# Optimization experiments

Measured on AMD Instinct MI355X. Metric: run time of the kernel, lower is better.

The kernel has to match this reference:

```python
import jax, jax.numpy as jnp
import numpy as np

EPS = 1e-7  # keras K.epsilon()


def setup_inputs() -> dict:
    key = jax.random.key(0)
    k1, k2, k3, k4 = jax.random.split(key, 4)
    B, Lc, La, Dc, Da = 64, 512, 64, 1024, 1024
    return {
        "context": jax.random.normal(k1, (B, Lc, Dc), dtype=jnp.float32),
        "asp_text": jax.random.normal(k2, (B, La, Da), dtype=jnp.float32),
        "context_w": jax.random.normal(k3, (Dc, Da), dtype=jnp.float32) / np.sqrt(Dc),
        "context_b": jnp.zeros((Lc,), dtype=jnp.float32),
        "aspect_w": jax.random.normal(k4, (Da, Dc), dtype=jnp.float32) / np.sqrt(Da),
        "aspect_b": jnp.zeros((La,), dtype=jnp.float32),
    }


def reference(context, asp_text, context_w, context_b, aspect_w, aspect_b):
    # context: [B, Lc, Dc], asp_text: [B, La, Da]
    context_avg = jnp.mean(context, axis=1)   # [B, Dc]
    asp_avg = jnp.mean(asp_text, axis=1)      # [B, Da]

    # context attention scored against mean-pooled aspect
    s_c = jnp.einsum('bld,de,be->bl', context, context_w, asp_avg)  # [B, Lc]
    a_c = jnp.exp(jnp.tanh(s_c + context_b))
    a_c = a_c / (jnp.sum(a_c, axis=1, keepdims=True) + EPS)
    attend_context = jnp.einsum('bld,bl->bd', context, a_c)         # [B, Dc]

    # aspect attention scored against mean-pooled context
    s_t = jnp.einsum('bld,de,be->bl', asp_text, aspect_w, context_avg)  # [B, La]
    a_t = jnp.exp(jnp.tanh(s_t + aspect_b))
    # NOTE: faithful to original code's bug -- a_t is REPLACED by its sum
    # (not normalized), so the aspect branch scales sum(asp_text) by a scalar.
    a_t_sum = jnp.sum(a_t, axis=1, keepdims=True) + EPS              # [B, 1]
    attend_asp = jnp.sum(asp_text * a_t_sum[..., None], axis=1)      # [B, Da]

    return jnp.concatenate([attend_context, attend_asp], axis=-1)    # [B, Dc+Da]
```

## Files before the change

kernel.cpp:

```cpp
#include <hip/hip_runtime.h>
#include <hip/hip_bf16.h>

#define EPS 1e-7f

#define B   64
#define LC  512
#define LA  64
#define D   1024
#define D4  256
#define ROWS 16
#define CCHUNKS (LC / ROWS)

__global__ void k_asp_psum(const float* __restrict__ A, float* __restrict__ P) {
    int b = blockIdx.y, s = blockIdx.x, t = threadIdx.x;
    const float4* Ab = reinterpret_cast<const float4*>(A + (size_t)b * LA * D);
    float sx = 0.f, sy = 0.f, sz = 0.f, sw = 0.f;
    #pragma unroll
    for (int r = 0; r < ROWS; ++r) {
        float4 v = Ab[(s * ROWS + r) * D4 + t];
        sx += v.x; sy += v.y; sz += v.z; sw += v.w;
    }
    float4 o; o.x = sx; o.y = sy; o.z = sz; o.w = sw;
    reinterpret_cast<float4*>(P)[(b * 4 + s) * D4 + t] = o;
}

__global__ void k_asp_combine(const float* __restrict__ P, float* __restrict__ avg) {
    int b = blockIdx.x, t = threadIdx.x;
    const float4* P4 = reinterpret_cast<const float4*>(P);
    float sx = 0.f, sy = 0.f, sz = 0.f, sw = 0.f;
    #pragma unroll
    for (int s = 0; s < 4; ++s) {
        float4 v = P4[(b * 4 + s) * D4 + t];
        sx += v.x; sy += v.y; sz += v.z; sw += v.w;
    }
    const float inv = 1.0f / (float)LA;
    float4 o; o.x = sx * inv; o.y = sy * inv; o.z = sz * inv; o.w = sw * inv;
    reinterpret_cast<float4*>(avg)[b * D4 + t] = o;
}

__global__ void k_matvec(const float* __restrict__ W, const float* __restrict__ X,
                         float* __restrict__ V) {
    int w    = threadIdx.x >> 6;
    int lane = threadIdx.x & 63;
    int d0   = (blockIdx.x * 4 + w) * 2;
    int b0   = blockIdx.y * 16;

    float4 w0[4], w1[4];
    const float4* Wr0 = reinterpret_cast<const float4*>(W + (size_t)d0 * D);
    const float4* Wr1 = reinterpret_cast<const float4*>(W + (size_t)(d0 + 1) * D);
    #pragma unroll
    for (int k = 0; k < 4; ++k) { w0[k] = Wr0[lane + 64 * k]; w1[k] = Wr1[lane + 64 * k]; }

    #pragma unroll 4
    for (int bb = 0; bb < 16; ++bb) {
        int b = b0 + bb;
        const float4* Xr = reinterpret_cast<const float4*>(X + (size_t)b * D);
        float p0 = 0.f, p1 = 0.f;
        #pragma unroll
        for (int k = 0; k < 4; ++k) {
            float4 x = Xr[lane + 64 * k];
            p0 += x.x * w0[k].x + x.y * w0[k].y + x.z * w0[k].z + x.w * w0[k].w;
            p1 += x.x * w1[k].x + x.y * w1[k].y + x.z * w1[k].z + x.w * w1[k].w;
        }
        #pragma unroll
        for (int m = 1; m < 64; m <<= 1) {
            p0 += __shfl_xor(p0, m, 64);
            p1 += __shfl_xor(p1, m, 64);
        }
        if (lane == 0) { V[b * D + d0] = p0; V[b * D + d0 + 1] = p1; }
    }
}

__global__ __launch_bounds__(256, 4)
void k_ctx_pass(const float* __restrict__ C, const float* __restrict__ vc,
                const float* __restrict__ cb,
                float* __restrict__ pacc, float* __restrict__ psum,
                float* __restrict__ pesum) {
    __shared__ float sdot[ROWS][4];
    __shared__ float se[ROWS];
    int b = blockIdx.y, c = blockIdx.x;
    int w    = threadIdx.x >> 6;
    int lane = threadIdx.x & 63;
    int f4   = w * 64 + lane;

    float4 vr = reinterpret_cast<const float4*>(vc + (size_t)b * D)[f4];

    const float4* Cb = reinterpret_cast<const float4*>(C + ((size_t)b * LC + c * ROWS) * D);
    float4 x[ROWS];
    #pragma unroll
    for (int r = 0; r < ROWS; ++r) x[r] = Cb[r * D4 + f4];

    #pragma unroll
    for (int r = 0; r < ROWS; ++r) {
        float p = x[r].x * vr.x + x[r].y * vr.y + x[r].z * vr.z + x[r].w * vr.w;
        #pragma unroll
        for (int m = 1; m < 64; m <<= 1) p += __shfl_xor(p, m, 64);
        if (lane == 0) sdot[r][w] = p;
    }
    __syncthreads();
    if (threadIdx.x < ROWS) {
        int r = threadIdx.x;
        float s = sdot[r][0] + sdot[r][1] + sdot[r][2] + sdot[r][3];
        se[r] = expf(tanhf(s + cb[c * ROWS + r]));
    }
    __syncthreads();

    float4 acc = {0.f, 0.f, 0.f, 0.f}, sct = {0.f, 0.f, 0.f, 0.f};
    #pragma unroll
    for (int r = 0; r < ROWS; ++r) {
        float e = se[r];
        acc.x += e * x[r].x; acc.y += e * x[r].y; acc.z += e * x[r].z; acc.w += e * x[r].w;
        sct.x += x[r].x;     sct.y += x[r].y;     sct.z += x[r].z;     sct.w += x[r].w;
    }
    int pidx = b * CCHUNKS + c;
    reinterpret_cast<float4*>(pacc)[pidx * D4 + f4] = acc;
    reinterpret_cast<float4*>(psum)[pidx * D4 + f4] = sct;
    if (w == 0) {
        float e2 = (lane < ROWS) ? se[lane] : 0.f;
        #pragma unroll
        for (int m = 1; m < 64; m <<= 1) e2 += __shfl_xor(e2, m, 64);
        if (lane == 0) pesum[pidx] = e2;
    }
}

__global__ void k_ctx_reduce(const float* __restrict__ pacc, const float* __restrict__ psum,
                             const float* __restrict__ pesum,
                             float* __restrict__ out, float* __restrict__ ctx_avg) {
    int b = blockIdx.y, q = blockIdx.x;
    int f4 = q * 64 + threadIdx.x;
    float ax = 0.f, ay = 0.f, az = 0.f, aw = 0.f;
    float sx = 0.f, sy = 0.f, sz = 0.f, sw = 0.f;
    const float4* pa = reinterpret_cast<const float4*>(pacc);
    const float4* ps = reinterpret_cast<const float4*>(psum);
    #pragma unroll 8
    for (int c = 0; c < CCHUNKS; ++c) {
        float4 va = pa[(b * CCHUNKS + c) * D4 + f4];
        float4 vs = ps[(b * CCHUNKS + c) * D4 + f4];
        ax += va.x; ay += va.y; az += va.z; aw += va.w;
        sx += vs.x; sy += vs.y; sz += vs.z; sw += vs.w;
    }
    float es = 0.f;
    #pragma unroll 8
    for (int c = 0; c < CCHUNKS; ++c) es += pesum[b * CCHUNKS + c];
    float inv = 1.0f / (es + EPS);
    float4 o; o.x = ax * inv; o.y = ay * inv; o.z = az * inv; o.w = aw * inv;
    reinterpret_cast<float4*>(out)[b * (2 * D4) + f4] = o;
    const float invL = 1.0f / (float)LC;
    float4 m; m.x = sx * invL; m.y = sy * invL; m.z = sz * invL; m.w = sw * invL;
    reinterpret_cast<float4*>(ctx_avg)[b * D4 + f4] = m;
}

__global__ void k_asp_score(const float* __restrict__ A, const float* __restrict__ vt,
                            const float* __restrict__ ab, float* __restrict__ pesumA) {
    __shared__ float sdot[ROWS][4];
    __shared__ float se[ROWS];
    int b = blockIdx.y, q = blockIdx.x;
    int w    = threadIdx.x >> 6;
    int lane = threadIdx.x & 63;
    int f4   = w * 64 + lane;

    float4 vr = reinterpret_cast<const float4*>(vt + (size_t)b * D)[f4];
    const float4* Ab = reinterpret_cast<const float4*>(A + ((size_t)b * LA + q * ROWS) * D);
    #pragma unroll
    for (int r = 0; r < ROWS; ++r) {
        float4 x = Ab[r * D4 + f4];
        float p = x.x * vr.x + x.y * vr.y + x.z * vr.z + x.w * vr.w;
        #pragma unroll
        for (int m = 1; m < 64; m <<= 1) p += __shfl_xor(p, m, 64);
        if (lane == 0) sdot[r][w] = p;
    }
    __syncthreads();
    if (threadIdx.x < ROWS) {
        int r = threadIdx.x;
        float s = sdot[r][0] + sdot[r][1] + sdot[r][2] + sdot[r][3];
        se[r] = expf(tanhf(s + ab[q * ROWS + r]));
    }
    __syncthreads();
    if (w == 0) {
        float e2 = (lane < ROWS) ? se[lane] : 0.f;
        #pragma unroll
        for (int m = 1; m < 64; m <<= 1) e2 += __shfl_xor(e2, m, 64);
        if (lane == 0) pesumA[b * 4 + q] = e2;
    }
}

__global__ void k_asp_scale(const float* __restrict__ pesumA, const float* __restrict__ asp_avg,
                            float* __restrict__ out) {
    int b = blockIdx.x, t = threadIdx.x;
    float es = pesumA[b * 4 + 0] + pesumA[b * 4 + 1] + pesumA[b * 4 + 2] + pesumA[b * 4 + 3];
    float scale = (es + EPS) * (float)LA;
    float4 av = reinterpret_cast<const float4*>(asp_avg)[b * D4 + t];
    float4 o; o.x = av.x * scale; o.y = av.y * scale; o.z = av.z * scale; o.w = av.w * scale;
    reinterpret_cast<float4*>(out)[b * (2 * D4) + D4 + t] = o;
}

extern "C" void kernel_launch(void* const* d_in, const int* in_sizes, int n_in,
                              void* d_out, int out_size, void* d_ws, size_t ws_size,
                              hipStream_t stream) {
    const float* context   = (const float*)d_in[0];
    const float* asp_text  = (const float*)d_in[1];
    const float* context_w = (const float*)d_in[2];
    const float* context_b = (const float*)d_in[3];
    const float* aspect_w  = (const float*)d_in[4];
    const float* aspect_b  = (const float*)d_in[5];
    float* out = (float*)d_out;
    float* ws  = (float*)d_ws;

    float* asp_avg = ws;
    float* v_c     = asp_avg + B * D;
    float* ctx_avg = v_c + B * D;
    float* v_t     = ctx_avg + B * D;
    float* pacc    = v_t + B * D;
    float* psum    = pacc + (size_t)B * CCHUNKS * D;
    float* pesum   = psum + (size_t)B * CCHUNKS * D;
    float* pesumA  = pesum + B * CCHUNKS;
    float* Ppart   = pesumA + B * 4;

    k_asp_psum   <<<dim3(4, B),  256, 0, stream>>>(asp_text, Ppart);
    k_asp_combine<<<B,           256, 0, stream>>>(Ppart, asp_avg);
    k_matvec     <<<dim3(128, 4),256, 0, stream>>>(context_w, asp_avg, v_c);
    k_ctx_pass   <<<dim3(CCHUNKS, B), 256, 0, stream>>>(context, v_c, context_b,
                                                        pacc, psum, pesum);
    k_ctx_reduce <<<dim3(4, B),  64,  0, stream>>>(pacc, psum, pesum, out, ctx_avg);
    k_matvec     <<<dim3(128, 4),256, 0, stream>>>(aspect_w, ctx_avg, v_t);
    k_asp_score  <<<dim3(4, B),  256, 0, stream>>>(asp_text, v_t, aspect_b, pesumA);
    k_asp_scale  <<<B,           256, 0, stream>>>(pesumA, asp_avg, out);
}
```

Baseline: 264.6 us.

## Fuse aspect-average combine into matvec and halve context-pass partial blocks

Measured after the change: 291.2 us. +10.0%, slower.

```diff
diff --git a/kernel.cpp b/kernel.cpp
--- a/kernel.cpp
+++ b/kernel.cpp
@@ -9,7 +9,8 @@
 #define D   1024
 #define D4  256
 #define ROWS 16
-#define CCHUNKS (LC / ROWS)
+#define HALVES 2
+#define CCH  (LC / (ROWS * HALVES))
 
 __global__ void k_asp_psum(const float* __restrict__ A, float* __restrict__ P) {
     int b = blockIdx.y, s = blockIdx.x, t = threadIdx.x;
@@ -24,20 +25,7 @@
     reinterpret_cast<float4*>(P)[(b * 4 + s) * D4 + t] = o;
 }
 
-__global__ void k_asp_combine(const float* __restrict__ P, float* __restrict__ avg) {
-    int b = blockIdx.x, t = threadIdx.x;
-    const float4* P4 = reinterpret_cast<const float4*>(P);
-    float sx = 0.f, sy = 0.f, sz = 0.f, sw = 0.f;
-    #pragma unroll
-    for (int s = 0; s < 4; ++s) {
-        float4 v = P4[(b * 4 + s) * D4 + t];
-        sx += v.x; sy += v.y; sz += v.z; sw += v.w;
-    }
-    const float inv = 1.0f / (float)LA;
-    float4 o; o.x = sx * inv; o.y = sy * inv; o.z = sz * inv; o.w = sw * inv;
-    reinterpret_cast<float4*>(avg)[b * D4 + t] = o;
-}
-
+template <int COMBINE>
 __global__ void k_matvec(const float* __restrict__ W, const float* __restrict__ X,
                          float* __restrict__ V) {
     int w    = threadIdx.x >> 6;
@@ -54,11 +42,23 @@
     #pragma unroll 4
     for (int bb = 0; bb < 16; ++bb) {
         int b = b0 + bb;
-        const float4* Xr = reinterpret_cast<const float4*>(X + (size_t)b * D);
         float p0 = 0.f, p1 = 0.f;
         #pragma unroll
         for (int k = 0; k < 4; ++k) {
-            float4 x = Xr[lane + 64 * k];
+            float4 x;
+            if (COMBINE) {
+                const float4* P4 = reinterpret_cast<const float4*>(X);
+                float4 a0 = P4[(b * 4 + 0) * D4 + lane + 64 * k];
+                float4 a1 = P4[(b * 4 + 1) * D4 + lane + 64 * k];
+                float4 a2 = P4[(b * 4 + 2) * D4 + lane + 64 * k];
+                float4 a3 = P4[(b * 4 + 3) * D4 + lane + 64 * k];
+                x.x = a0.x + a1.x + a2.x + a3.x;
+                x.y = a0.y + a1.y + a2.y + a3.y;
+                x.z = a0.z + a1.z + a2.z + a3.z;
+                x.w = a0.w + a1.w + a2.w + a3.w;
+            } else {
+                x = reinterpret_cast<const float4*>(X + (size_t)b * D)[lane + 64 * k];
+            }
             p0 += x.x * w0[k].x + x.y * w0[k].y + x.z * w0[k].z + x.w * w0[k].w;
             p1 += x.x * w1[k].x + x.y * w1[k].y + x.z * w1[k].z + x.w * w1[k].w;
         }
@@ -67,7 +67,10 @@
             p0 += __shfl_xor(p0, m, 64);
             p1 += __shfl_xor(p1, m, 64);
         }
-        if (lane == 0) { V[b * D + d0] = p0; V[b * D + d0 + 1] = p1; }
+        if (lane == 0) {
+            const float s = COMBINE ? (1.0f / (float)LA) : 1.0f;
+            V[b * D + d0] = p0 * s; V[b * D + d0 + 1] = p1 * s;
+        }
     }
 }
 
@@ -76,8 +79,8 @@
                 const float* __restrict__ cb,
                 float* __restrict__ pacc, float* __restrict__ psum,
                 float* __restrict__ pesum) {
-    __shared__ float sdot[ROWS][4];
-    __shared__ float se[ROWS];
+    __shared__ float sdot[HALVES][ROWS][4];
+    __shared__ float se[HALVES][ROWS];
     int b = blockIdx.y, c = blockIdx.x;
     int w    = threadIdx.x >> 6;
     int lane = threadIdx.x & 63;
@@ -85,38 +88,50 @@
 
     float4 vr = reinterpret_cast<const float4*>(vc + (size_t)b * D)[f4];
 
-    const float4* Cb = reinterpret_cast<const float4*>(C + ((size_t)b * LC + c * ROWS) * D);
-    float4 x[ROWS];
-    #pragma unroll
-    for (int r = 0; r < ROWS; ++r) x[r] = Cb[r * D4 + f4];
-
-    #pragma unroll
-    for (int r = 0; r < ROWS; ++r) {
-        float p = x[r].x * vr.x + x[r].y * vr.y + x[r].z * vr.z + x[r].w * vr.w;
-        #pragma unroll
-        for (int m = 1; m < 64; m <<= 1) p += __shfl_xor(p, m, 64);
-        if (lane == 0) sdot[r][w] = p;
-    }
-    __syncthreads();
-    if (threadIdx.x < ROWS) {
-        int r = threadIdx.x;
-        float s = sdot[r][0] + sdot[r][1] + sdot[r][2] + sdot[r][3];
-        se[r] = expf(tanhf(s + cb[c * ROWS + r]));
-    }
-    __syncthreads();
-
     float4 acc = {0.f, 0.f, 0.f, 0.f}, sct = {0.f, 0.f, 0.f, 0.f};
-    #pragma unroll
-    for (int r = 0; r < ROWS; ++r) {
-        float e = se[r];
-        acc.x += e * x[r].x; acc.y += e * x[r].y; acc.z += e * x[r].z; acc.w += e * x[r].w;
-        sct.x += x[r].x;     sct.y += x[r].y;     sct.z += x[r].z;     sct.w += x[r].w;
-    }
-    int pidx = b * CCHUNKS + c;
+    float es_local = 0.f;
+
+    const float4* Cb0 = reinterpret_cast<const float4*>(
+        C + ((size_t)b * LC + (size_t)c * ROWS * HALVES) * D);
+
+    #pragma unroll
+    for (int h = 0; h < HALVES; ++h) {
+        const float4* Cb = Cb0 + (size_t)h * ROWS * D4;
+        float4 x[ROWS];
+        #pragma unroll
+        for (int r = 0; r < ROWS; ++r) x[r] = Cb[r * D4 + f4];
+
+        #pragma unroll
+        for (int r = 0; r < ROWS; ++r) {
+            float p = x[r].x * vr.x + x[r].y * vr.y + x[r].z * vr.z + x[r].w * vr.w;
+            #pragma unroll
+            for (int m = 1; m < 64; m <<= 1) p += __shfl_xor(p, m, 64);
+            if (lane == 0) sdot[h][r][w] = p;
+        }
+        __syncthreads();
+        if (threadIdx.x < ROWS) {
+            int r = threadIdx.x;
+            float s = sdot[h][r][0] + sdot[h][r][1] + sdot[h][r][2] + sdot[h][r][3];
+            float e = expf(tanhf(s + cb[(c * HALVES + h) * ROWS + r]));
+            se[h][r] = e;
+            es_local += e;
+        }
+        __syncthreads();
+        #pragma unroll
+        for (int r = 0; r < ROWS; ++r) {
+            float e = se[h][r];
+            acc.x += e * x[r].x; acc.y += e * x[r].y;
+            acc.z += e * x[r].z; acc.w += e * x[r].w;
+            sct.x += x[r].x;     sct.y += x[r].y;
+            sct.z += x[r].z;     sct.w += x[r].w;
+        }
+    }
+
+    int pidx = b * CCH + c;
     reinterpret_cast<float4*>(pacc)[pidx * D4 + f4] = acc;
     reinterpret_cast<float4*>(psum)[pidx * D4 + f4] = sct;
     if (w == 0) {
-        float e2 = (lane < ROWS) ? se[lane] : 0.f;
+        float e2 = (lane < ROWS) ? es_local : 0.f;
         #pragma unroll
         for (int m = 1; m < 64; m <<= 1) e2 += __shfl_xor(e2, m, 64);
         if (lane == 0) pesum[pidx] = e2;
@@ -132,16 +147,16 @@
     float sx = 0.f, sy = 0.f, sz = 0.f, sw = 0.f;
     const float4* pa = reinterpret_cast<const float4*>(pacc);
     const float4* ps = reinterpret_cast<const float4*>(psum);
-    #pragma unroll 8
-    for (int c = 0; c < CCHUNKS; ++c) {
-        float4 va = pa[(b * CCHUNKS + c) * D4 + f4];
-        float4 vs = ps[(b * CCHUNKS + c) * D4 + f4];
+    #pragma unroll
+    for (int c = 0; c < CCH; ++c) {
+        float4 va = pa[(b * CCH + c) * D4 + f4];
+        float4 vs = ps[(b * CCH + c) * D4 + f4];
         ax += va.x; ay += va.y; az += va.z; aw += va.w;
         sx += vs.x; sy += vs.y; sz += vs.z; sw += vs.w;
     }
     float es = 0.f;
-    #pragma unroll 8
-    for (int c = 0; c < CCHUNKS; ++c) es += pesum[b * CCHUNKS + c];
+    #pragma unroll
+    for (int c = 0; c < CCH; ++c) es += pesum[b * CCH + c];
     float inv = 1.0f / (es + EPS);
     float4 o; o.x = ax * inv; o.y = ay * inv; o.z = az * inv; o.w = aw * inv;
     reinterpret_cast<float4*>(out)[b * (2 * D4) + f4] = o;
@@ -184,13 +199,21 @@
     }
 }
 
-__global__ void k_asp_scale(const float* __restrict__ pesumA, const float* __restrict__ asp_avg,
+__global__ void k_asp_scale(const float* __restrict__ pesumA, const float* __restrict__ P,
                             float* __restrict__ out) {
     int b = blockIdx.x, t = threadIdx.x;
     float es = pesumA[b * 4 + 0] + pesumA[b * 4 + 1] + pesumA[b * 4 + 2] + pesumA[b * 4 + 3];
-    float scale = (es + EPS) * (float)LA;
-    float4 av = reinterpret_cast<const float4*>(asp_avg)[b * D4 + t];
-    float4 o; o.x = av.x * scale; o.y = av.y * scale; o.z = av.z * scale; o.w = av.w * scale;
+    float scale = es + EPS;
+    const float4* P4 = reinterpret_cast<const float4*>(P);
+    float4 a0 = P4[(b * 4 + 0) * D4 + t];
+    float4 a1 = P4[(b * 4 + 1) * D4 + t];
+    float4 a2 = P4[(b * 4 + 2) * D4 + t];
+    float4 a3 = P4[(b * 4 + 3) * D4 + t];
+    float4 o;
+    o.x = (a0.x + a1.x + a2.x + a3.x) * scale;
+    o.y = (a0.y + a1.y + a2.y + a3.y) * scale;
+    o.z = (a0.z + a1.z + a2.z + a3.z) * scale;
+    o.w = (a0.w + a1.w + a2.w + a3.w) * scale;
     reinterpret_cast<float4*>(out)[b * (2 * D4) + D4 + t] = o;
 }
 
@@ -206,23 +229,21 @@
     float* out = (float*)d_out;
     float* ws  = (float*)d_ws;
 
-    float* asp_avg = ws;
-    float* v_c     = asp_avg + B * D;
+    float* v_c     = ws;
     float* ctx_avg = v_c + B * D;
     float* v_t     = ctx_avg + B * D;
-    float* pacc    = v_t + B * D;
-    float* psum    = pacc + (size_t)B * CCHUNKS * D;
-    float* pesum   = psum + (size_t)B * CCHUNKS * D;
-    float* pesumA  = pesum + B * CCHUNKS;
-    float* Ppart   = pesumA + B * 4;
-
-    k_asp_psum   <<<dim3(4, B),  256, 0, stream>>>(asp_text, Ppart);
-    k_asp_combine<<<B,           256, 0, stream>>>(Ppart, asp_avg);
-    k_matvec     <<<dim3(128, 4),256, 0, stream>>>(context_w, asp_avg, v_c);
-    k_ctx_pass   <<<dim3(CCHUNKS, B), 256, 0, stream>>>(context, v_c, context_b,
-                                                        pacc, psum, pesum);
-    k_ctx_reduce <<<dim3(4, B),  64,  0, stream>>>(pacc, psum, pesum, out, ctx_avg);
-    k_matvec     <<<dim3(128, 4),256, 0, stream>>>(aspect_w, ctx_avg, v_t);
-    k_asp_score  <<<dim3(4, B),  256, 0, stream>>>(asp_text, v_t, aspect_b, pesumA);
-    k_asp_scale  <<<B,           256, 0, stream>>>(pesumA, asp_avg, out);
-}
+    float* Ppart   = v_t + B * D;
+    float* pacc    = Ppart + 4 * B * D;
+    float* psum    = pacc + (size_t)B * CCH * D;
+    float* pesum   = psum + (size_t)B * CCH * D;
+    float* pesumA  = pesum + B * CCH;
+
+    k_asp_psum   <<<dim3(4, B),   256, 0, stream>>>(asp_text, Ppart);
+    k_matvec<1>  <<<dim3(128, 4), 256, 0, stream>>>(context_w, Ppart, v_c);
+    k_ctx_pass   <<<dim3(CCH, B), 256, 0, stream>>>(context, v_c, context_b,
+                                                    pacc, psum, pesum);
+    k_ctx_reduce <<<dim3(4, B),   64,  0, stream>>>(pacc, psum, pesum, out, ctx_avg);
+    k_matvec<0>  <<<dim3(128, 4), 256, 0, stream>>>(aspect_w, ctx_avg, v_t);
+    k_asp_score  <<<dim3(4, B),   256, 0, stream>>>(asp_text, v_t, aspect_b, pesumA);
+    k_asp_scale  <<<B,            256, 0, stream>>>(pesumA, Ppart, out);
+}
```
